# Kernel tuning notes

Measured on AMD Instinct MI355X. Metric: run time of the kernel, lower is better.

## Reference

```python
import jax, jax.numpy as jnp
import numpy as np
from jax import lax

NL = 32            # number of ocean layers
NFORCING = 720     # hourly forcing steps (30 days)
DT_FORCING = 3600.0
DT = 60.0
NSUB = 60          # dt_forcing // dt
FC_VAL = 1e-4      # Coriolis frequency [s^-1]


def setup_inputs() -> dict:
    key = jax.random.key(0)
    k1, k2, k3 = jax.random.split(key, 3)
    # pk = log(K); keep K in a physically sane range via offset
    pk = jax.random.normal(k1, (2 * NL,), dtype=jnp.float32) * 0.5 - 10.0
    TAx = jax.random.normal(k2, (NFORCING,), dtype=jnp.float32) * 0.1  # wind stress [N/m^2]
    TAy = jax.random.normal(k3, (NFORCING,), dtype=jnp.float32) * 0.1
    fc = jnp.full((1,), FC_VAL, dtype=jnp.float32)
    return {"pk": pk, "TAx": TAx, "TAy": TAy, "fc": fc}


def _vector_field(t, U, V, f, K, TAx, TAy):
    # temporal interpolation of forcing (matches original index arithmetic)
    it = jnp.asarray(t // DT, jnp.int32)
    itf = it // NSUB
    aa = (jnp.mod(it, NSUB) / NSUB).astype(U.dtype)
    nT = TAx.shape[0]
    itsup = jnp.where(itf + 1 >= nT, -1, itf + 1)
    TAxnow = (1 - aa) * TAx[itf] + aa * TAx[itsup]
    TAynow = (1 - aa) * TAy[itf] + aa * TAy[itsup]
    # N-layer stencil (nl > 1 branch of lax.cond), fully vectorized:
    #   layer 0   : +Kin[0]*TA       - Kout[0]*(x0 - x1)
    #   layer k   : -Kin[k]*(xk-xk-1) - Kout[k]*(xk - xk+1)
    #   layer nl-1: -Kin[-1]*(x - x_prev) - Kout[-1]*x   (i.e. x_next = 0)
    Kin, Kout = K[0::2], K[1::2]                       # [nl] each
    zero = jnp.zeros((1,), U.dtype)
    Unext = jnp.concatenate([U[1:], zero])
    Vnext = jnp.concatenate([V[1:], zero])
    dU_top = jnp.concatenate([Kin[:1] * TAxnow, -Kin[1:] * (U[1:] - U[:-1])])
    dV_top = jnp.concatenate([Kin[:1] * TAynow, -Kin[1:] * (V[1:] - V[:-1])])
    d_U = f * V + dU_top - Kout * (U - Unext)
    d_V = -f * U + dV_top - Kout * (V - Vnext)
    return d_U, d_V


def reference(pk, TAx, TAy, fc):
    nl = pk.shape[0] // 2
    K = jnp.exp(pk)
    f = fc[0]
    Nforcing = TAx.shape[0]
    U0 = jnp.zeros((Nforcing, nl), dtype=pk.dtype)
    V0 = jnp.zeros((Nforcing, nl), dtype=pk.dtype)

    def inner(carry, iin):
        Uold, Vold, iout = carry
        t = iout * DT_FORCING + iin * DT
        d_U, d_V = _vector_field(t, Uold, Vold, f, K, TAx, TAy)
        return (Uold + DT * d_U, Vold + DT * d_V, iout), None

    def outer(carry, iout):
        U, V = carry
        (u, v, _), _ = lax.scan(inner, (U[iout], V[iout], iout),
                                jnp.arange(NSUB))
        # last write (iout+1 == Nforcing) is out-of-bounds -> dropped,
        # exactly as in the original .at[].set semantics
        U = U.at[iout + 1].set(u)
        V = V.at[iout + 1].set(v)
        return (U, V), None

    (U, V), _ = lax.scan(outer, (U0, V0), jnp.arange(Nforcing))
    return U, V
```

## Files before the change

### kernel.cpp

```cpp
#include <hip/hip_runtime.h>
#include <hip/hip_bf16.h>

#define NLAYERS 32
#define NFORC   720
#define NSUB    60
#define DTS     60.0f
#define T_CH    24
#define N_CH    30
#define MAGIC   0x1234ABCD
#define SD      34


__device__ __forceinline__ bool sniff_bf16(const void* pk_raw, int lane) {
    const __hip_bfloat16* pk_bf = (const __hip_bfloat16*)pk_raw;
    const float v = __bfloat162float(pk_bf[lane]);
    return __all(v > -30.0f && v < -1.0f);
}

__device__ __forceinline__ void load_mrow(const float2* sMat, int i, int h, float2* R) {
    const float4* rp = (const float4*)(sMat + i * SD + h * 16);
    #pragma unroll
    for (int jj = 0; jj < 8; ++jj) {
        const float4 v = rp[jj];
        R[2 * jj]     = make_float2(v.x, v.y);
        R[2 * jj + 1] = make_float2(v.z, v.w);
    }
}

__device__ __forceinline__ float2 rmatvec(const float2* R, float2 x, int hbase) {
    float a0 = 0.f, a1 = 0.f, a2 = 0.f, a3 = 0.f;
    #pragma unroll
    for (int jj = 0; jj < 16; ++jj) {
        const float xr = __shfl(x.x, hbase + jj);
        const float xi = __shfl(x.y, hbase + jj);
        const float2 m = R[jj];
        a0 = fmaf(m.x, xr, a0);
        a1 = fmaf(m.y, xi, a1);
        a2 = fmaf(m.x, xi, a2);
        a3 = fmaf(m.y, xr, a3);
    }
    float yr = a0 - a1, yi = a2 + a3;
    yr += __shfl_xor(yr, 32);
    yi += __shfl_xor(yi, 32);
    return make_float2(yr, yi);
}

__device__ __forceinline__ float2 rmatvec_lds(const float2* mat, float2 x,
                                              int l, int h, int hbase) {
    float2 R[16];
    load_mrow(mat, l, h, R);
    return rmatvec(R, x, hbase);
}

__device__ __forceinline__ void cmatmul8(float2* D, const float2* A, const float2* B, int tt) {
    const int i = tt >> 2, j0 = (tt & 3) * 8;
    float ar[8], ai[8];
    #pragma unroll
    for (int m = 0; m < 8; ++m) { ar[m] = 0.f; ai[m] = 0.f; }
    #pragma unroll 4
    for (int k = 0; k < 32; ++k) {
        const float2 a = A[i * SD + k];
        const float4* bp = (const float4*)(B + k * SD + j0);
        #pragma unroll
        for (int m = 0; m < 4; ++m) {
            const float4 b = bp[m];
            ar[2*m]   = fmaf(a.x, b.x, fmaf(-a.y, b.y, ar[2*m]));
            ai[2*m]   = fmaf(a.x, b.y, fmaf( a.y, b.x, ai[2*m]));
            ar[2*m+1] = fmaf(a.x, b.z, fmaf(-a.y, b.w, ar[2*m+1]));
            ai[2*m+1] = fmaf(a.x, b.w, fmaf( a.y, b.z, ai[2*m+1]));
        }
    }
    float4* dp = (float4*)(D + i * SD + j0);
    #pragma unroll
    for (int m = 0; m < 4; ++m)
        dp[m] = make_float4(ar[2*m], ai[2*m], ar[2*m+1], ai[2*m+1]);
}

__device__ __forceinline__ void lds_wait_ge(int* p, int target) {
    while (__hip_atomic_load(p, __ATOMIC_ACQUIRE, __HIP_MEMORY_SCOPE_WORKGROUP) < target)
        __builtin_amdgcn_s_sleep(8);
}

__global__ __launch_bounds__(1024, 1)
void junsteak_one(const void* pk_raw, const void* tax_raw, const void* tay_raw,
                  const void* fc_raw, float2* ws_z, int* ws_flag, void* out_raw)
{
    __shared__ __align__(16) float2 sM  [NLAYERS * SD];
    __shared__ __align__(16) float2 sL2 [NLAYERS * SD];
    __shared__ __align__(16) float2 sL4 [NLAYERS * SD];
    __shared__ __align__(16) float2 sL8 [NLAYERS * SD];
    __shared__ __align__(16) float2 sL16[NLAYERS * SD];
    __shared__ __align__(16) float2 sE  [NLAYERS * SD];
    __shared__ __align__(16) float2 sCX [NFORC];
    __shared__ __align__(16) float2 sP1 [T_CH * NLAYERS];
    __shared__ __align__(16) float2 sZL [(N_CH - 1) * NLAYERS];
    __shared__ __align__(16) float2 sBC [NLAYERS];
    __shared__ __align__(16) float4 sPQ [NLAYERS];
    __shared__ int sLad, sZrdy, sBrdy;

    const int t = threadIdx.x, lane = t & 63, wv = t >> 6;
    const int l = lane & 31, h = lane >> 5, col = 2 * wv + h;
    const int c = blockIdx.x;
    const int hbase = 16 * h;

    if (t == 0) { sLad = 0; sZrdy = 0; sBrdy = 0; }

    const bool bf = sniff_bf16(pk_raw, lane);

    float kin, kout, f, dtkin0;
    if (bf) {
        const __hip_bfloat16* pk = (const __hip_bfloat16*)pk_raw;
        kin    = expf(__bfloat162float(pk[2 * l]));
        kout   = expf(__bfloat162float(pk[2 * l + 1]));
        f      = __bfloat162float(((const __hip_bfloat16*)fc_raw)[0]);
        dtkin0 = DTS * expf(__bfloat162float(pk[0]));
        const __hip_bfloat16* tx = (const __hip_bfloat16*)tax_raw;
        const __hip_bfloat16* ty = (const __hip_bfloat16*)tay_raw;
        if (t < NFORC)
            sCX[t] = make_float2(__bfloat162float(tx[t]), __bfloat162float(ty[t]));
    } else {
        const float* pk = (const float*)pk_raw;
        kin    = expf(pk[2 * l]);
        kout   = expf(pk[2 * l + 1]);
        f      = ((const float*)fc_raw)[0];
        dtkin0 = DTS * expf(pk[0]);
        const float* tx = (const float*)tax_raw;
        const float* ty = (const float*)tay_raw;
        if (t < NFORC) sCX[t] = make_float2(tx[t], ty[t]);
    }

    __hip_bfloat16* out_bf = (__hip_bfloat16*)out_raw;
    float*          out_f  = (float*)out_raw;
    const int VOFF = NFORC * NLAYERS;

    if (c == 0 && t < 64) {
        const int off = (t >= 32 ? VOFF : 0) + (t & 31);
        if (bf) out_bf[off] = __float2bfloat16(0.0f); else out_f[off] = 0.0f;
    }

    {
        float xr = (l == col) ? 1.0f : 0.0f, xi = 0.0f;
        float Pr = 0.f, Pi = 0.f, Qr = 0.f, Qi = 0.f;
        const bool row0 = (l == 0), row31 = (l == 31);
        for (int m = 0; m < NSUB; ++m) {
            const float cp = dtkin0 * (float)(m + 1) * (1.0f / 60.0f);
            const float cq = dtkin0 * (float)(NSUB - 1 - m) * (1.0f / 60.0f);
            Pr = fmaf(cp, xr, Pr); Pi = fmaf(cp, xi, Pi);
            Qr = fmaf(cq, xr, Qr); Qi = fmaf(cq, xi, Qi);
            float xrm = __shfl_up(xr, 1);
            float xim = __shfl_up(xi, 1);
            float xrp = __shfl_down(xr, 1);
            float xip = __shfl_down(xi, 1);
            if (row31) { xrp = 0.0f; xip = 0.0f; }
            const float Lr = row0 ? (-kout * (xr - xrp))
                                  : (-kin * (xr - xrm) - kout * (xr - xrp));
            const float Li = row0 ? (-kout * (xi - xip))
                                  : (-kin * (xi - xim) - kout * (xi - xip));
            const float nxr = xr + DTS * Lr + DTS * f * xi;
            const float nxi = xi + DTS * Li - DTS * f * xr;
            xr = nxr; xi = nxi;
        }
        sM[l * SD + col] = make_float2(xr, xi);
        if (wv == 0 && h == 0) sPQ[l] = make_float4(Pr, Pi, Qr, Qi);
    }
    __syncthreads();

    const int a      = c * T_CH;
    const int bend   = min(a + T_CH, NFORC - 1);
    const int nsteps = bend - a;
    float2 x = make_float2(0.0f, 0.0f);

    if (wv == 0) {
        const float4 pq = sPQ[l];
        float2 Mreg[16];
        load_mrow(sM, l, h, Mreg);
        float2 cn = sCX[a];
        for (int s = a; s < bend; ++s) {
            const float2 cs = cn;
            cn = sCX[s + 1];
            const float2 y = rmatvec(Mreg, x, hbase);
            const float gr = pq.x * cs.x - pq.y * cs.y + pq.z * cn.x - pq.w * cn.y;
            const float gi = pq.x * cs.y + pq.y * cs.x + pq.z * cn.y + pq.w * cn.x;
            x = make_float2(y.x + gr, y.y + gi);
            if (h == 0) sP1[(s - a) * NLAYERS + l] = x;
        }
        if (h == 0) {
            unsigned long long zu;
            __builtin_memcpy(&zu, &x, 8);
            __hip_atomic_store((unsigned long long*)(ws_z + c * NLAYERS + l), zu,
                               __ATOMIC_RELAXED, __HIP_MEMORY_SCOPE_AGENT);
        }
        __threadfence();
        if (lane == 0)
            __hip_atomic_store(ws_flag + c, (int)MAGIC,
                               __ATOMIC_RELEASE, __HIP_MEMORY_SCOPE_AGENT);

        lds_wait_ge(&sLad, 10);
        lds_wait_ge(&sZrdy, 1);

        float2 Ereg[16];
        load_mrow(sE, l, h, Ereg);
        x = make_float2(0.0f, 0.0f);
        for (int j = 0; j < c; ++j) {
            const float2 z = sZL[j * NLAYERS + l];
            const float2 y = rmatvec(Ereg, x, hbase);
            x = make_float2(y.x + z.x, y.y + z.y);
        }
        if (h == 0) sBC[l] = x;
        if (lane == 0)
            __hip_atomic_store(&sBrdy, 1, __ATOMIC_RELEASE, __HIP_MEMORY_SCOPE_WORKGROUP);
    } else if (wv == 1 || wv == 2) {
        const int tt = t - 64;
        cmatmul8(sL2,  sM,  sM,  tt);
        if (lane == 0) __hip_atomic_fetch_add(&sLad, 1, __ATOMIC_ACQ_REL, __HIP_MEMORY_SCOPE_WORKGROUP);
        lds_wait_ge(&sLad, 2);
        cmatmul8(sL4,  sL2, sL2, tt);
        if (lane == 0) __hip_atomic_fetch_add(&sLad, 1, __ATOMIC_ACQ_REL, __HIP_MEMORY_SCOPE_WORKGROUP);
        lds_wait_ge(&sLad, 4);
        cmatmul8(sL8,  sL4, sL4, tt);
        if (lane == 0) __hip_atomic_fetch_add(&sLad, 1, __ATOMIC_ACQ_REL, __HIP_MEMORY_SCOPE_WORKGROUP);
        lds_wait_ge(&sLad, 6);
        cmatmul8(sL16, sL8, sL8, tt);
        if (lane == 0) __hip_atomic_fetch_add(&sLad, 1, __ATOMIC_ACQ_REL, __HIP_MEMORY_SCOPE_WORKGROUP);
        lds_wait_ge(&sLad, 8);
        cmatmul8(sE,   sL16, sL8, tt);
        if (lane == 0) __hip_atomic_fetch_add(&sLad, 1, __ATOMIC_ACQ_REL, __HIP_MEMORY_SCOPE_WORKGROUP);
    } else if (wv == 3) {
        if (c > 0) {
            int v;
            do {
                v = (lane < c) ? __hip_atomic_load(ws_flag + lane, __ATOMIC_ACQUIRE,
                                                   __HIP_MEMORY_SCOPE_AGENT)
                               : (int)MAGIC;
                if (!__all(v == (int)MAGIC)) __builtin_amdgcn_s_sleep(8);
                else break;
            } while (true);
            for (int idx = lane; idx < c * NLAYERS; idx += 64) {
                const unsigned long long zu =
                    __hip_atomic_load((const unsigned long long*)(ws_z + idx),
                                      __ATOMIC_RELAXED, __HIP_MEMORY_SCOPE_AGENT);
                float2 z;
                __builtin_memcpy(&z, &zu, 8);
                sZL[idx] = z;
            }
        }
        if (lane == 0)
            __hip_atomic_store(&sZrdy, 1, __ATOMIC_RELEASE, __HIP_MEMORY_SCOPE_WORKGROUP);
    }

    if (wv != 0) lds_wait_ge(&sBrdy, 1);

    const float2 b = (wv == 0) ? x : sBC[l];

    float2 corr = b;
    {
        const int e = wv + 1;
        if (e & 1)  corr = rmatvec_lds(sM,   corr, l, h, hbase);
        if (e & 2)  corr = rmatvec_lds(sL2,  corr, l, h, hbase);
        if (e & 4)  corr = rmatvec_lds(sL4,  corr, l, h, hbase);
        if (e & 8)  corr = rmatvec_lds(sL8,  corr, l, h, hbase);
        if (e & 16) corr = rmatvec_lds(sL16, corr, l, h, hbase);
    }
    if (wv < nsteps && h == 0) {
        const float2 st = sP1[wv * NLAYERS + l];
        const int row = (a + wv + 1) * NLAYERS + l;
        const float u = st.x + corr.x, vv = st.y + corr.y;
        if (bf) { out_bf[row] = __float2bfloat16(u); out_bf[VOFF + row] = __float2bfloat16(vv); }
        else    { out_f[row] = u;                    out_f[VOFF + row] = vv; }
    }
    const int m2 = wv + 16;
    if (m2 < T_CH) {
        corr = rmatvec_lds(sL16, corr, l, h, hbase);
        if (m2 < nsteps && h == 0) {
            const float2 st = sP1[m2 * NLAYERS + l];
            const int row = (a + m2 + 1) * NLAYERS + l;
            const float u = st.x + corr.x, vv = st.y + corr.y;
            if (bf) { out_bf[row] = __float2bfloat16(u); out_bf[VOFF + row] = __float2bfloat16(vv); }
            else    { out_f[row] = u;                    out_f[VOFF + row] = vv; }
        }
    }
}

extern "C" void kernel_launch(void* const* d_in, const int* in_sizes, int n_in,
                              void* d_out, int out_size, void* d_ws, size_t ws_size,
                              hipStream_t stream) {
    (void)in_sizes; (void)n_in; (void)out_size; (void)ws_size;
    float2* ws_z   = (float2*)d_ws;
    int*    ws_flg = (int*)((char*)d_ws + (size_t)N_CH * NLAYERS * sizeof(float2));
    junsteak_one<<<dim3(N_CH), dim3(1024), 0, stream>>>(
        d_in[0], d_in[1], d_in[2], d_in[3], ws_z, ws_flg, d_out);
}
```

Baseline: 101.5 us.

## Rechunk scan into 32-step chunks with readlane matvec and DPP stencil

```diff
diff --git a/kernel.cpp b/kernel.cpp
--- a/kernel.cpp
+++ b/kernel.cpp
@@ -5,11 +5,23 @@
 #define NFORC   720
 #define NSUB    60
 #define DTS     60.0f
-#define T_CH    24
-#define N_CH    30
+#define T_CH    32
+#define N_CH    23
 #define MAGIC   0x1234ABCD
 #define SD      34
 
+
+__device__ __forceinline__ float rl_f(float v, int j) {
+    return __int_as_float(__builtin_amdgcn_readlane(__float_as_int(v), j));
+}
+__device__ __forceinline__ float dpp_shr1(float v) {
+    return __int_as_float(__builtin_amdgcn_update_dpp(
+        0, __float_as_int(v), 0x111, 0xF, 0xF, true));
+}
+__device__ __forceinline__ float dpp_shl1(float v) {
+    return __int_as_float(__builtin_amdgcn_update_dpp(
+        0, __float_as_int(v), 0x101, 0xF, 0xF, true));
+}
 
 __device__ __forceinline__ bool sniff_bf16(const void* pk_raw, int lane) {
     const __hip_bfloat16* pk_bf = (const __hip_bfloat16*)pk_raw;
@@ -17,39 +29,29 @@
     return __all(v > -30.0f && v < -1.0f);
 }
 
-__device__ __forceinline__ void load_mrow(const float2* sMat, int i, int h, float2* R) {
-    const float4* rp = (const float4*)(sMat + i * SD + h * 16);
-    #pragma unroll
-    for (int jj = 0; jj < 8; ++jj) {
-        const float4 v = rp[jj];
-        R[2 * jj]     = make_float2(v.x, v.y);
-        R[2 * jj + 1] = make_float2(v.z, v.w);
-    }
-}
-
-__device__ __forceinline__ float2 rmatvec(const float2* R, float2 x, int hbase) {
+__device__ __forceinline__ void load_rows(const float2* mat, int q, float2* R) {
+    const float4* rp = (const float4*)(mat + q * SD);
+    #pragma unroll
+    for (int j = 0; j < 16; ++j) {
+        const float4 v = rp[j];
+        R[2 * j]     = make_float2(v.x, v.y);
+        R[2 * j + 1] = make_float2(v.z, v.w);
+    }
+}
+
+__device__ __forceinline__ float2 rlmatvec(const float2* R, float2 x) {
     float a0 = 0.f, a1 = 0.f, a2 = 0.f, a3 = 0.f;
     #pragma unroll
-    for (int jj = 0; jj < 16; ++jj) {
-        const float xr = __shfl(x.x, hbase + jj);
-        const float xi = __shfl(x.y, hbase + jj);
-        const float2 m = R[jj];
-        a0 = fmaf(m.x, xr, a0);
-        a1 = fmaf(m.y, xi, a1);
-        a2 = fmaf(m.x, xi, a2);
-        a3 = fmaf(m.y, xr, a3);
-    }
-    float yr = a0 - a1, yi = a2 + a3;
-    yr += __shfl_xor(yr, 32);
-    yi += __shfl_xor(yi, 32);
-    return make_float2(yr, yi);
-}
-
-__device__ __forceinline__ float2 rmatvec_lds(const float2* mat, float2 x,
-                                              int l, int h, int hbase) {
-    float2 R[16];
-    load_mrow(mat, l, h, R);
-    return rmatvec(R, x, hbase);
+    for (int j = 0; j < 32; ++j) {
+        const float bx = rl_f(x.x, j);
+        const float by = rl_f(x.y, j);
+        const float2 m = R[j];
+        a0 = fmaf(m.x, bx, a0);
+        a1 = fmaf(m.y, by, a1);
+        a2 = fmaf(m.x, by, a2);
+        a3 = fmaf(m.y, bx, a3);
+    }
+    return make_float2(a0 - a1, a2 + a3);
 }
 
 __device__ __forceinline__ void cmatmul8(float2* D, const float2* A, const float2* B, int tt) {
@@ -78,10 +80,10 @@
 
 __device__ __forceinline__ void lds_wait_ge(int* p, int target) {
     while (__hip_atomic_load(p, __ATOMIC_ACQUIRE, __HIP_MEMORY_SCOPE_WORKGROUP) < target)
-        __builtin_amdgcn_s_sleep(8);
-}
-
-__global__ __launch_bounds__(1024, 1)
+        __builtin_amdgcn_s_sleep(2);
+}
+
+__global__ __launch_bounds__(512, 2)
 void junsteak_one(const void* pk_raw, const void* tax_raw, const void* tay_raw,
                   const void* fc_raw, float2* ws_z, int* ws_flag, void* out_raw)
 {
@@ -99,34 +101,30 @@
     __shared__ int sLad, sZrdy, sBrdy;
 
     const int t = threadIdx.x, lane = t & 63, wv = t >> 6;
-    const int l = lane & 31, h = lane >> 5, col = 2 * wv + h;
+    const int q = lane & 31;
     const int c = blockIdx.x;
-    const int hbase = 16 * h;
 
     if (t == 0) { sLad = 0; sZrdy = 0; sBrdy = 0; }
 
     const bool bf = sniff_bf16(pk_raw, lane);
 
-    float kin, kout, f, dtkin0;
+    float f, dtkin0;
     if (bf) {
         const __hip_bfloat16* pk = (const __hip_bfloat16*)pk_raw;
-        kin    = expf(__bfloat162float(pk[2 * l]));
-        kout   = expf(__bfloat162float(pk[2 * l + 1]));
         f      = __bfloat162float(((const __hip_bfloat16*)fc_raw)[0]);
         dtkin0 = DTS * expf(__bfloat162float(pk[0]));
         const __hip_bfloat16* tx = (const __hip_bfloat16*)tax_raw;
         const __hip_bfloat16* ty = (const __hip_bfloat16*)tay_raw;
-        if (t < NFORC)
-            sCX[t] = make_float2(__bfloat162float(tx[t]), __bfloat162float(ty[t]));
+        for (int i = t; i < NFORC; i += 512)
+            sCX[i] = make_float2(__bfloat162float(tx[i]), __bfloat162float(ty[i]));
     } else {
         const float* pk = (const float*)pk_raw;
-        kin    = expf(pk[2 * l]);
-        kout   = expf(pk[2 * l + 1]);
         f      = ((const float*)fc_raw)[0];
         dtkin0 = DTS * expf(pk[0]);
         const float* tx = (const float*)tax_raw;
         const float* ty = (const float*)tay_raw;
-        if (t < NFORC) sCX[t] = make_float2(tx[t], ty[t]);
+        for (int i = t; i < NFORC; i += 512)
+            sCX[i] = make_float2(tx[i], ty[i]);
     }
 
     __hip_bfloat16* out_bf = (__hip_bfloat16*)out_raw;
@@ -138,30 +136,73 @@
         if (bf) out_bf[off] = __float2bfloat16(0.0f); else out_f[off] = 0.0f;
     }
 
-    {
-        float xr = (l == col) ? 1.0f : 0.0f, xi = 0.0f;
-        float Pr = 0.f, Pi = 0.f, Qr = 0.f, Qi = 0.f;
-        const bool row0 = (l == 0), row31 = (l == 31);
+    if (wv < 4) {
+        const int col = 8 * wv + (lane >> 3);
+        const int g   = lane & 7;
+        float kinr[4], koutr[4];
+        #pragma unroll
+        for (int r = 0; r < 4; ++r) {
+            const int R = 4 * g + r;
+            if (bf) {
+                const __hip_bfloat16* pk = (const __hip_bfloat16*)pk_raw;
+                kinr[r]  = expf(__bfloat162float(pk[2 * R]));
+                koutr[r] = expf(__bfloat162float(pk[2 * R + 1]));
+            } else {
+                const float* pk = (const float*)pk_raw;
+                kinr[r]  = expf(pk[2 * R]);
+                koutr[r] = expf(pk[2 * R + 1]);
+            }
+        }
+        float xr[4], xi[4], Pr[4], Pi[4], Qr[4], Qi[4];
+        #pragma unroll
+        for (int r = 0; r < 4; ++r) {
+            xr[r] = (4 * g + r == col) ? 1.0f : 0.0f;
+            xi[r] = 0.0f;
+            Pr[r] = Pi[r] = Qr[r] = Qi[r] = 0.0f;
+        }
+        const float dtf = DTS * f;
         for (int m = 0; m < NSUB; ++m) {
-            const float cp = dtkin0 * (float)(m + 1) * (1.0f / 60.0f);
-            const float cq = dtkin0 * (float)(NSUB - 1 - m) * (1.0f / 60.0f);
-            Pr = fmaf(cp, xr, Pr); Pi = fmaf(cp, xi, Pi);
-            Qr = fmaf(cq, xr, Qr); Qi = fmaf(cq, xi, Qi);
-            float xrm = __shfl_up(xr, 1);
-            float xim = __shfl_up(xi, 1);
-            float xrp = __shfl_down(xr, 1);
-            float xip = __shfl_down(xi, 1);
-            if (row31) { xrp = 0.0f; xip = 0.0f; }
-            const float Lr = row0 ? (-kout * (xr - xrp))
-                                  : (-kin * (xr - xrm) - kout * (xr - xrp));
-            const float Li = row0 ? (-kout * (xi - xip))
-                                  : (-kin * (xi - xim) - kout * (xi - xip));
-            const float nxr = xr + DTS * Lr + DTS * f * xi;
-            const float nxi = xi + DTS * Li - DTS * f * xr;
-            xr = nxr; xi = nxi;
-        }
-        sM[l * SD + col] = make_float2(xr, xi);
-        if (wv == 0 && h == 0) sPQ[l] = make_float4(Pr, Pi, Qr, Qi);
+            if (wv == 0) {
+                const float cp = dtkin0 * (float)(m + 1) * (1.0f / 60.0f);
+                const float cq = dtkin0 * (float)(NSUB - 1 - m) * (1.0f / 60.0f);
+                #pragma unroll
+                for (int r = 0; r < 4; ++r) {
+                    Pr[r] = fmaf(cp, xr[r], Pr[r]); Pi[r] = fmaf(cp, xi[r], Pi[r]);
+                    Qr[r] = fmaf(cq, xr[r], Qr[r]); Qi[r] = fmaf(cq, xi[r], Qi[r]);
+                }
+            }
+            float topr = dpp_shr1(xr[3]), topi = dpp_shr1(xi[3]);
+            float botr = dpp_shl1(xr[0]), boti = dpp_shl1(xi[0]);
+            if (g == 7) { botr = 0.0f; boti = 0.0f; }
+            float nxr[4], nxi[4];
+            #pragma unroll
+            for (int r = 0; r < 4; ++r) {
+                const float xmr = (r == 0) ? topr : xr[r - 1];
+                const float xmi = (r == 0) ? topi : xi[r - 1];
+                const float xpr = (r == 3) ? botr : xr[r + 1];
+                const float xpi = (r == 3) ? boti : xi[r + 1];
+                float Lr, Li;
+                if (r == 0 && g == 0) {
+                    Lr = -koutr[0] * (xr[0] - xpr);
+                    Li = -koutr[0] * (xi[0] - xpi);
+                } else {
+                    Lr = fmaf(-kinr[r], xr[r] - xmr, -koutr[r] * (xr[r] - xpr));
+                    Li = fmaf(-kinr[r], xi[r] - xmi, -koutr[r] * (xi[r] - xpi));
+                }
+                nxr[r] = fmaf(DTS, Lr, fmaf( dtf, xi[r], xr[r]));
+                nxi[r] = fmaf(DTS, Li, fmaf(-dtf, xr[r], xi[r]));
+            }
+            #pragma unroll
+            for (int r = 0; r < 4; ++r) { xr[r] = nxr[r]; xi[r] = nxi[r]; }
+        }
+        #pragma unroll
+        for (int r = 0; r < 4; ++r)
+            sM[(4 * g + r) * SD + col] = make_float2(xr[r], xi[r]);
+        if (wv == 0 && lane < 8) {
+            #pragma unroll
+            for (int r = 0; r < 4; ++r)
+                sPQ[4 * g + r] = make_float4(Pr[r], Pi[r], Qr[r], Qi[r]);
+        }
     }
     __syncthreads();
 
@@ -171,23 +212,23 @@
     float2 x = make_float2(0.0f, 0.0f);
 
     if (wv == 0) {
-        const float4 pq = sPQ[l];
-        float2 Mreg[16];
-        load_mrow(sM, l, h, Mreg);
+        float2 RM[32];
+        load_rows(sM, q, RM);
+        const float4 pq = sPQ[q];
         float2 cn = sCX[a];
         for (int s = a; s < bend; ++s) {
             const float2 cs = cn;
             cn = sCX[s + 1];
-            const float2 y = rmatvec(Mreg, x, hbase);
+            const float2 y = rlmatvec(RM, x);
             const float gr = pq.x * cs.x - pq.y * cs.y + pq.z * cn.x - pq.w * cn.y;
             const float gi = pq.x * cs.y + pq.y * cs.x + pq.z * cn.y + pq.w * cn.x;
             x = make_float2(y.x + gr, y.y + gi);
-            if (h == 0) sP1[(s - a) * NLAYERS + l] = x;
-        }
-        if (h == 0) {
+            if (lane < 32) sP1[(s - a) * NLAYERS + q] = x;
+        }
+        if (lane < 32) {
             unsigned long long zu;
             __builtin_memcpy(&zu, &x, 8);
-            __hip_atomic_store((unsigned long long*)(ws_z + c * NLAYERS + l), zu,
+            __hip_atomic_store((unsigned long long*)(ws_z + c * NLAYERS + q), zu,
                                __ATOMIC_RELAXED, __HIP_MEMORY_SCOPE_AGENT);
         }
         __threadfence();
@@ -198,32 +239,32 @@
         lds_wait_ge(&sLad, 10);
         lds_wait_ge(&sZrdy, 1);
 
-        float2 Ereg[16];
-        load_mrow(sE, l, h, Ereg);
+        float2 RE[32];
+        load_rows(sE, q, RE);
         x = make_float2(0.0f, 0.0f);
         for (int j = 0; j < c; ++j) {
-            const float2 z = sZL[j * NLAYERS + l];
-            const float2 y = rmatvec(Ereg, x, hbase);
+            const float2 z = sZL[j * NLAYERS + q];
+            const float2 y = rlmatvec(RE, x);
             x = make_float2(y.x + z.x, y.y + z.y);
         }
-        if (h == 0) sBC[l] = x;
+        if (lane < 32) sBC[q] = x;
         if (lane == 0)
             __hip_atomic_store(&sBrdy, 1, __ATOMIC_RELEASE, __HIP_MEMORY_SCOPE_WORKGROUP);
     } else if (wv == 1 || wv == 2) {
         const int tt = t - 64;
-        cmatmul8(sL2,  sM,  sM,  tt);
+        cmatmul8(sL2,  sM,   sM,   tt);
         if (lane == 0) __hip_atomic_fetch_add(&sLad, 1, __ATOMIC_ACQ_REL, __HIP_MEMORY_SCOPE_WORKGROUP);
         lds_wait_ge(&sLad, 2);
-        cmatmul8(sL4,  sL2, sL2, tt);
+        cmatmul8(sL4,  sL2,  sL2,  tt);
         if (lane == 0) __hip_atomic_fetch_add(&sLad, 1, __ATOMIC_ACQ_REL, __HIP_MEMORY_SCOPE_WORKGROUP);
         lds_wait_ge(&sLad, 4);
-        cmatmul8(sL8,  sL4, sL4, tt);
+        cmatmul8(sL8,  sL4,  sL4,  tt);
         if (lane == 0) __hip_atomic_fetch_add(&sLad, 1, __ATOMIC_ACQ_REL, __HIP_MEMORY_SCOPE_WORKGROUP);
         lds_wait_ge(&sLad, 6);
-        cmatmul8(sL16, sL8, sL8, tt);
+        cmatmul8(sL16, sL8,  sL8,  tt);
         if (lane == 0) __hip_atomic_fetch_add(&sLad, 1, __ATOMIC_ACQ_REL, __HIP_MEMORY_SCOPE_WORKGROUP);
         lds_wait_ge(&sLad, 8);
-        cmatmul8(sE,   sL16, sL8, tt);
+        cmatmul8(sE,   sL16, sL16, tt);
         if (lane == 0) __hip_atomic_fetch_add(&sLad, 1, __ATOMIC_ACQ_REL, __HIP_MEMORY_SCOPE_WORKGROUP);
     } else if (wv == 3) {
         if (c > 0) {
@@ -232,8 +273,8 @@
                 v = (lane < c) ? __hip_atomic_load(ws_flag + lane, __ATOMIC_ACQUIRE,
                                                    __HIP_MEMORY_SCOPE_AGENT)
                                : (int)MAGIC;
-                if (!__all(v == (int)MAGIC)) __builtin_amdgcn_s_sleep(8);
-                else break;
+                if (__all(v == (int)MAGIC)) break;
+                __builtin_amdgcn_s_sleep(2);
             } while (true);
             for (int idx = lane; idx < c * NLAYERS; idx += 64) {
                 const unsigned long long zu =
@@ -249,34 +290,34 @@
     }
 
     if (wv != 0) lds_wait_ge(&sBrdy, 1);
-
-    const float2 b = (wv == 0) ? x : sBC[l];
-
-    float2 corr = b;
-    {
-        const int e = wv + 1;
-        if (e & 1)  corr = rmatvec_lds(sM,   corr, l, h, hbase);
-        if (e & 2)  corr = rmatvec_lds(sL2,  corr, l, h, hbase);
-        if (e & 4)  corr = rmatvec_lds(sL4,  corr, l, h, hbase);
-        if (e & 8)  corr = rmatvec_lds(sL8,  corr, l, h, hbase);
-        if (e & 16) corr = rmatvec_lds(sL16, corr, l, h, hbase);
-    }
-    if (wv < nsteps && h == 0) {
-        const float2 st = sP1[wv * NLAYERS + l];
-        const int row = (a + wv + 1) * NLAYERS + l;
-        const float u = st.x + corr.x, vv = st.y + corr.y;
-        if (bf) { out_bf[row] = __float2bfloat16(u); out_bf[VOFF + row] = __float2bfloat16(vv); }
-        else    { out_f[row] = u;                    out_f[VOFF + row] = vv; }
-    }
-    const int m2 = wv + 16;
-    if (m2 < T_CH) {
-        corr = rmatvec_lds(sL16, corr, l, h, hbase);
-        if (m2 < nsteps && h == 0) {
-            const float2 st = sP1[m2 * NLAYERS + l];
-            const int row = (a + m2 + 1) * NLAYERS + l;
-            const float u = st.x + corr.x, vv = st.y + corr.y;
-            if (bf) { out_bf[row] = __float2bfloat16(u); out_bf[VOFF + row] = __float2bfloat16(vv); }
-            else    { out_f[row] = u;                    out_f[VOFF + row] = vv; }
+    const float2 b = (wv == 0) ? x : sBC[q];
+
+    float2 R2[32];
+    float2 cur = b;
+    const int e0 = wv + 1;
+    if (e0 & 1) { load_rows(sM,  q, R2); cur = rlmatvec(R2, cur); }
+    if (e0 & 2) { load_rows(sL2, q, R2); cur = rlmatvec(R2, cur); }
+    if (e0 & 4) { load_rows(sL4, q, R2); cur = rlmatvec(R2, cur); }
+    if (e0 & 8) { load_rows(sL8, q, R2); cur = rlmatvec(R2, cur); }
+    #pragma unroll
+    for (int k = 0; k < 4; ++k) {
+        if (k > 0) {
+            if (k == 1 && !(e0 & 8)) load_rows(sL8, q, R2);
+            cur = rlmatvec(R2, cur);
+        }
+        const int m = wv + 8 * k;
+        if (m < nsteps && lane < 32) {
+            const float2 st = sP1[m * NLAYERS + q];
+            const float u  = st.x + cur.x;
+            const float vv = st.y + cur.y;
+            const int row = (a + m + 1) * NLAYERS + q;
+            if (bf) {
+                out_bf[row]        = __float2bfloat16(u);
+                out_bf[VOFF + row] = __float2bfloat16(vv);
+            } else {
+                out_f[row]        = u;
+                out_f[VOFF + row] = vv;
+            }
         }
     }
 }
@@ -287,6 +328,6 @@
     (void)in_sizes; (void)n_in; (void)out_size; (void)ws_size;
     float2* ws_z   = (float2*)d_ws;
     int*    ws_flg = (int*)((char*)d_ws + (size_t)N_CH * NLAYERS * sizeof(float2));
-    junsteak_one<<<dim3(N_CH), dim3(1024), 0, stream>>>(
+    junsteak_one<<<dim3(N_CH), dim3(512), 0, stream>>>(
         d_in[0], d_in[1], d_in[2], d_in[3], ws_z, ws_flg, d_out);
 }
```

New measurement: 96.15 us. 5.2% less time.
